# Kernel optimization log

Measured on AMD Instinct MI355X. Metric: run time of the kernel, lower is better.

## Reference

```python
import jax, jax.numpy as jnp
import numpy as np

B, T, C, H, W = 16, 8, 16, 64, 64
HID = 32          # round(sqrt(num_audio_input_ch * num_latent_ch)) = sqrt(16*64)
LAT = 64          # num_latent_ch
K = 3             # kernel_size


def conv(x, w, b):
    # x: [B,Cin,H,W], w: [Cout,Cin,K,K] (OIHW), SAME padding == padding (1,1) for 3x3
    y = jax.lax.conv_general_dilated(x, w, (1, 1), 'SAME',
                                     dimension_numbers=('NCHW', 'OIHW', 'NCHW'))
    return y + b[None, :, None, None]


def lstm_scan(x_seq, w, b, hid):
    # x_seq: [T,B,Cin,H,W] -> hidden sequence [T,B,hid,H,W]
    Bn, Hh, Ww = x_seq.shape[1], x_seq.shape[3], x_seq.shape[4]
    h0 = jnp.zeros((Bn, hid, Hh, Ww), x_seq.dtype)

    def step(carry, x_t):
        h, c = carry
        z = conv(jnp.concatenate([x_t, h], axis=1), w, b)     # [B,4*hid,H,W]
        i, f, o, g = jnp.split(z, 4, axis=1)                   # gate order i,f,o,g
        c2 = jax.nn.sigmoid(f) * c + jax.nn.sigmoid(i) * jnp.tanh(g)
        h2 = jax.nn.sigmoid(o) * jnp.tanh(c2)
        return (h2, c2), h2

    _, hs = jax.lax.scan(step, (h0, h0), x_seq)
    return hs


def bidir_layer(x_seq, wf, bf, wb, bb, hid):
    hf = lstm_scan(x_seq, wf, bf, hid)
    hb = jnp.flip(lstm_scan(jnp.flip(x_seq, 0), wb, bb, hid), 0)
    return jnp.concatenate([hf, hb], axis=2)                   # [T,B,2*hid,H,W]


def setup_inputs() -> dict:
    key = jax.random.key(0)
    ks = jax.random.split(key, 16)
    s = 0.05
    pe_dim = C * H * W
    inp = {
        'x_audio': jax.random.normal(ks[0], (B, T, C, H, W), jnp.float32),
        'midi_notes': jax.random.uniform(ks[1], (B, T, 2), jnp.float32, 0.0, 127.0),
        # note encoder: Linear(2,4) -> ReLU -> Linear(4, C*H*W) -> Tanh
        'enc_w1': jax.random.normal(ks[2], (2, 4), jnp.float32) * s,
        'enc_b1': jnp.zeros((4,), jnp.float32),
        'enc_w2': jax.random.normal(ks[3], (4, pe_dim), jnp.float32) * s,
        'enc_b2': jnp.zeros((pe_dim,), jnp.float32),
        # layer 0 (input C=16), fwd + bwd cells
        'w0f': jax.random.normal(ks[4], (4 * HID, C + HID, K, K), jnp.float32) * s,
        'b0f': jnp.zeros((4 * HID,), jnp.float32),
        'w0b': jax.random.normal(ks[5], (4 * HID, C + HID, K, K), jnp.float32) * s,
        'b0b': jnp.zeros((4 * HID,), jnp.float32),
        # layer 1 (input 2*HID=64)
        'w1f': jax.random.normal(ks[6], (4 * HID, 2 * HID + HID, K, K), jnp.float32) * s,
        'b1f': jnp.zeros((4 * HID,), jnp.float32),
        'w1b': jax.random.normal(ks[7], (4 * HID, 2 * HID + HID, K, K), jnp.float32) * s,
        'b1b': jnp.zeros((4 * HID,), jnp.float32),
        # final conv: 2*HID -> LAT
        'fc_w': jax.random.normal(ks[8], (LAT, 2 * HID, K, K), jnp.float32) * s,
        'fc_b': jnp.zeros((LAT,), jnp.float32),
    }
    return inp


def reference(x_audio, midi_notes, enc_w1, enc_b1, enc_w2, enc_b2,
              w0f, b0f, w0b, b0b, w1f, b1f, w1b, b1b, fc_w, fc_b):
    # positional encoding from MIDI notes, vectorized over all timesteps
    notes = -0.5 + midi_notes / 64.0                              # [B,T,2]
    pe = jnp.tanh(jax.nn.relu(notes @ enc_w1 + enc_b1) @ enc_w2 + enc_b2)  # [B,T,C*H*W]
    x = x_audio + pe.reshape(x_audio.shape)
    xs = jnp.transpose(x, (1, 0, 2, 3, 4))                        # [T,B,C,H,W]
    h = bidir_layer(xs, w0f, b0f, w0b, b0b, HID)                  # [T,B,64,H,W]
    h = bidir_layer(h, w1f, b1f, w1b, b1b, HID)                   # [T,B,64,H,W]
    return conv(h[-1], fc_w, fc_b)                                # [B,LAT,H,W]
```

## Files before the change

### kernel.cpp

```cpp
#include <hip/hip_runtime.h>

typedef _Float16 f16;
typedef _Float16 f16x8 __attribute__((ext_vector_type(8)));
typedef float f32x16 __attribute__((ext_vector_type(16)));

namespace {

constexpr int B_ = 16, T_ = 8, HW = 4096;

__device__ __forceinline__ float sigm(float x)  { return 1.f / (1.f + __expf(-x)); }
__device__ __forceinline__ float ftanh(float x) { return 1.f - 2.f / (1.f + __expf(2.f * x)); }

__device__ __forceinline__ f32x16 zero16() {
  f32x16 v;
#pragma unroll
  for (int i = 0; i < 16; ++i) v[i] = 0.f;
  return v;
}

struct WSet { const float* src; f16* dst; int KC, NCO, CIN; };

__global__ void warr_kernel(WSet s0, WSet s1, WSet s2, WSet s3, WSet s4) {
  WSet s = s0;
  switch (blockIdx.y) { case 1: s = s1; break; case 2: s = s2; break;
                        case 3: s = s3; break; case 4: s = s4; break; default: break; }
  int n = 9 * s.KC * s.NCO * 16;
  int i = blockIdx.x * 256 + threadIdx.x;
  if (i >= n) return;
  int kk = i & 15;
  int t = i >> 4;
  int co = t % s.NCO;
  int dkc = t / s.NCO;
  int kc = dkc % s.KC, dydx = dkc / s.KC;
  int ci = kc * 16 + kk;
  float v = (ci < s.CIN) ? s.src[(co * s.CIN + ci) * 9 + dydx] : 0.f;
  s.dst[i] = (f16)v;
}

__global__ void pe_kernel(const float* __restrict__ xa, const float* __restrict__ midi,
                          const float* __restrict__ w1, const float* __restrict__ b1,
                          const float* __restrict__ w2, const float* __restrict__ b2,
                          f16* __restrict__ xs) {
  int gid = blockIdx.x * 256 + threadIdx.x;
  int half = gid & 1;
  int gpx = gid >> 1;
  int bt = gpx >> 12, gp = gpx & 4095;
  float n0 = -0.5f + midi[bt * 2 + 0] * (1.f / 64.f);
  float n1 = -0.5f + midi[bt * 2 + 1] * (1.f / 64.f);
  float hk[4];
#pragma unroll
  for (int k = 0; k < 4; ++k)
    hk[k] = fmaxf(fmaf(n0, w1[k], fmaf(n1, w1[4 + k], b1[k])), 0.f);
  f16x8 ov;
#pragma unroll
  for (int j = 0; j < 8; ++j) {
    int c = half * 8 + j;
    long p = (long)c * HW + gp;
    float z = b2[p];
#pragma unroll
    for (int k = 0; k < 4; ++k) z = fmaf(hk[k], w2[(long)k * 65536 + p], z);
    ov[j] = (f16)(xa[(long)bt * 65536 + p] + ftanh(z));
  }
  *reinterpret_cast<f16x8*>(xs + (long)gpx * 16 + half * 8) = ov;
}

struct ConvDir {
  const f16* x;  long xbs;
  const f16* h;  long hbs;
  const f16* w;
  const float* bias;
  const float* cin;
  float* cout;
  f16* hout; long hobs;
};

template<int CIN1, int CIN2, int CINPAD, int KCF, int KC, int HST, int HOST,
         bool GATES, int NCO, int MG, int MFRAG>
__global__ __launch_bounds__(512, 4)
void conv_mfma(ConvDir p0, ConvDir p1)
{
  constexpr int NG = 8 / MG;
  constexpr int NF = NCO / (NG * 32);
  constexpr int ACT_BYTES = 180 * CINPAD * 2;
  constexpr int ZB_BYTES  = GATES ? 64 * 128 * 4 : 0;
  constexpr int SMEM = ACT_BYTES > ZB_BYTES ? ACT_BYTES : ZB_BYTES;
  __shared__ __align__(16) char smem[SMEM];
  f16*   act  = (f16*)smem;
  float* zbuf = (float*)smem;

  const ConvDir P = blockIdx.y ? p1 : p0;
  const int b = blockIdx.z;
  const int tileY = blockIdx.x >> 2, tileX = blockIdx.x & 3;
  const int gy0 = tileY * 8, gx0 = tileX * 16;
  const int tid = threadIdx.x;

  constexpr int UPX = CIN1 / 8, UPH = CIN2 / 8, UPP = UPX + UPH;
  const bool have_h = (P.h != nullptr);
  for (int i = tid; i < 180 * UPP; i += 512) {
    int px = i / UPP, u = i - px * UPP;
    if (u >= UPX && !have_h) continue;
    int py = px / 18, pxx = px - py * 18;
    int gy = gy0 + py - 1, gx = gx0 + pxx - 1;
    f16x8 v;
#pragma unroll
    for (int j = 0; j < 8; ++j) v[j] = (f16)0.f;
    if ((unsigned)gy < 64u && (unsigned)gx < 64u) {
      long gp = (long)gy * 64 + gx;
      const f16* src = (u < UPX) ? (P.x + b * P.xbs + gp * CIN1 + u * 8)
                                 : (P.h + b * P.hbs + gp * HST + (u - UPX) * 8);
      v = *reinterpret_cast<const f16x8*>(src);
    }
    *reinterpret_cast<f16x8*>(act + px * CINPAD + u * 8) = v;
  }
  __syncthreads();

  const int lane = tid & 63, wv = tid >> 6;
  const int mg = wv % MG, ng = wv / MG;
  const int rl = lane & 31;
  const int khalf = (lane >> 5) * 8;
  const int laneA = ((rl >> 4) * 18 + (rl & 15)) * CINPAD + khalf;
  const int laneB = rl * 16 + khalf;

  f32x16 acc[MFRAG][NF];
#pragma unroll
  for (int m = 0; m < MFRAG; ++m)
#pragma unroll
    for (int nf = 0; nf < NF; ++nf) acc[m][nf] = zero16();

  const f16* __restrict__ wng = P.w + laneB;
  const f16* __restrict__ arow = act + laneA;

#pragma unroll
  for (int dy = 0; dy < 3; ++dy)
#pragma unroll
  for (int dx = 0; dx < 3; ++dx) {
    const int dydx = dy * 3 + dx;
    f16x8 bf[KC][NF];
#pragma unroll
    for (int kc = 0; kc < KC; ++kc)
#pragma unroll
      for (int nf = 0; nf < NF; ++nf)
        bf[kc][nf] = *reinterpret_cast<const f16x8*>(
            wng + ((long)(dydx * KCF + kc) * NCO + (ng * NF + nf) * 32) * 16);
    f16x8 af[MFRAG][KC];
#pragma unroll
    for (int m = 0; m < MFRAG; ++m)
#pragma unroll
      for (int kc = 0; kc < KC; ++kc)
        af[m][kc] = *reinterpret_cast<const f16x8*>(
            arow + dx * CINPAD + (((mg * MFRAG + m) * 2 + dy) * 18) * CINPAD + kc * 16);
#pragma unroll
    for (int kc = 0; kc < KC; ++kc)
#pragma unroll
      for (int m = 0; m < MFRAG; ++m)
#pragma unroll
        for (int nf = 0; nf < NF; ++nf)
          acc[m][nf] = __builtin_amdgcn_mfma_f32_32x32x16_f16(af[m][kc], bf[kc][nf], acc[m][nf], 0, 0, 0);
  }

  __syncthreads();

  if constexpr (GATES) {
#pragma unroll
    for (int phase = 0; phase < 2; ++phase) {
      if (mg == phase) {
#pragma unroll
        for (int m = 0; m < MFRAG; ++m) {
#pragma unroll
          for (int nf = 0; nf < NF; ++nf) {
            const int col = (ng * NF + nf) * 32 + rl;
            const float bs = P.bias[col];
#pragma unroll
            for (int r = 0; r < 16; ++r) {
              int row = (r & 3) + 8 * (r >> 2) + 4 * (lane >> 5);
              zbuf[(m * 32 + row) * 128 + col] = acc[m][nf][r] + bs;
            }
          }
        }
      }
      __syncthreads();
      const int hid = tid & 31;
#pragma unroll
      for (int i = 0; i < 4; ++i) {
        int pl = (tid >> 5) + i * 16;
        int pxt = phase * 64 + pl;
        int py = pxt >> 4, pxx = pxt & 15;
        long gp = (long)(gy0 + py) * 64 + (gx0 + pxx);
        float zi = zbuf[pl * 128 + hid];
        float zf = zbuf[pl * 128 + 32 + hid];
        float zo = zbuf[pl * 128 + 64 + hid];
        float zg = zbuf[pl * 128 + 96 + hid];
        long cidx = ((long)b * HW + gp) * 32 + hid;
        float cp = P.cin ? P.cin[cidx] : 0.f;
        float c2 = sigm(zf) * cp + sigm(zi) * ftanh(zg);
        P.cout[cidx] = c2;
        P.hout[b * P.hobs + gp * HOST + hid] = (f16)(sigm(zo) * ftanh(c2));
      }
      __syncthreads();
    }
  } else {
#pragma unroll
    for (int m = 0; m < MFRAG; ++m) {
#pragma unroll
      for (int nf = 0; nf < NF; ++nf) {
        const int co = (ng * NF + nf) * 32 + rl;
        const float bs = P.bias[co];
#pragma unroll
        for (int r = 0; r < 16; ++r) {
          int row = (r & 3) + 8 * (r >> 2) + 4 * (lane >> 5);
          int pxt = (mg * MFRAG + m) * 32 + row;
          int py = pxt >> 4, pxx = pxt & 15;
          long gp = (long)(gy0 + py) * 64 + (gx0 + pxx);
          P.cout[((long)b * NCO + co) * HW + gp] = acc[m][nf][r] + bs;
        }
      }
    }
  }
}

}

extern "C" void kernel_launch(void* const* d_in, const int* in_sizes, int n_in,
                              void* d_out, int out_size, void* d_ws, size_t ws_size,
                              hipStream_t stream) {
  const float* x_audio = (const float*)d_in[0];
  const float* midi    = (const float*)d_in[1];
  const float* enc_w1  = (const float*)d_in[2];
  const float* enc_b1  = (const float*)d_in[3];
  const float* enc_w2  = (const float*)d_in[4];
  const float* enc_b2  = (const float*)d_in[5];
  const float* w0f = (const float*)d_in[6];
  const float* b0f = (const float*)d_in[7];
  const float* w0b = (const float*)d_in[8];
  const float* b0b = (const float*)d_in[9];
  const float* w1f = (const float*)d_in[10];
  const float* b1f = (const float*)d_in[11];
  const float* w1b = (const float*)d_in[12];
  const float* b1b = (const float*)d_in[13];
  const float* fcw = (const float*)d_in[14];
  const float* fcb = (const float*)d_in[15];

  char* ws = (char*)d_ws;
  size_t off = 0;
  auto alloc = [&](size_t bytes) { char* p = ws + off; off += (bytes + 255) & ~(size_t)255; return p; };

  f16* xs    = (f16*)alloc((size_t)B_ * T_ * HW * 16 * 2);
  f16* seq0  = (f16*)alloc((size_t)T_ * B_ * HW * 64 * 2);
  float* c0f = (float*)alloc((size_t)B_ * HW * 32 * 4);
  float* c0b = (float*)alloc((size_t)B_ * HW * 32 * 4);
  float* c1f = (float*)alloc((size_t)B_ * HW * 32 * 4);
  float* c1bw= (float*)alloc((size_t)B_ * HW * 32 * 4);
  f16* h1p0  = (f16*)alloc((size_t)B_ * HW * 32 * 2);
  f16* h1p1  = (f16*)alloc((size_t)B_ * HW * 32 * 2);
  f16* h1bw  = (f16*)alloc((size_t)B_ * HW * 32 * 2);
  f16* wt0f  = (f16*)alloc((size_t)9 * 3 * 128 * 16 * 2);
  f16* wt0b  = (f16*)alloc((size_t)9 * 3 * 128 * 16 * 2);
  f16* wt1f  = (f16*)alloc((size_t)9 * 6 * 128 * 16 * 2);
  f16* wt1b  = (f16*)alloc((size_t)9 * 6 * 128 * 16 * 2);
  f16* wtfc  = (f16*)alloc((size_t)9 * 4 * 64 * 16 * 2);

  {
    WSet s0{w0f, wt0f, 3, 128, 48}, s1{w0b, wt0b, 3, 128, 48};
    WSet s2{w1f, wt1f, 6, 128, 96}, s3{w1b, wt1b, 6, 128, 96};
    WSet s4{fcw, wtfc, 4, 64, 64};
    warr_kernel<<<dim3(432, 5), 256, 0, stream>>>(s0, s1, s2, s3, s4);
  }

  pe_kernel<<<(B_ * T_ * HW * 2) / 256, 256, 0, stream>>>(
      x_audio, midi, enc_w1, enc_b1, enc_w2, enc_b2, xs);

  const long XSB  = (long)T_ * HW * 16;
  const long SLAB = (long)B_ * HW * 64;
  const long SB   = (long)HW * 64;
  const long HB   = (long)HW * 32;

  {
    ConvDir f{xs, XSB, nullptr, SB, wt0f, b0f, nullptr, c0f, seq0, SB};
    ConvDir r{xs + (long)7 * HW * 16, XSB, nullptr, SB, wt0b, b0b, nullptr, c0b,
              seq0 + (long)7 * SLAB + 32, SB};
    conv_mfma<16, 32, 56, 3, 1, 64, 64, true, 128, 2, 2>
        <<<dim3(32, 2, 16), 512, 0, stream>>>(f, r);
  }
  for (int s = 1; s < 8; ++s) {
    int tf = s, tb = 7 - s;
    ConvDir f{xs + (long)tf * HW * 16, XSB,
              seq0 + (long)(tf - 1) * SLAB, SB,
              wt0f, b0f, c0f, c0f,
              seq0 + (long)tf * SLAB, SB};
    ConvDir r{xs + (long)tb * HW * 16, XSB,
              seq0 + (long)(tb + 1) * SLAB + 32, SB,
              wt0b, b0b, c0b, c0b,
              seq0 + (long)tb * SLAB + 32, SB};
    conv_mfma<16, 32, 56, 3, 3, 64, 64, true, 128, 2, 2>
        <<<dim3(32, 2, 16), 512, 0, stream>>>(f, r);
  }

  {
    ConvDir f{seq0, SB, nullptr, HB, wt1f, b1f, nullptr, c1f, h1p0, HB};
    ConvDir r{seq0 + 7 * SLAB, SB, nullptr, HB, wt1b, b1b, nullptr, c1bw, h1bw, HB};
    conv_mfma<64, 32, 104, 6, 4, 32, 32, true, 128, 2, 2>
        <<<dim3(32, 2, 16), 512, 0, stream>>>(f, r);
  }
  for (int s = 1; s < 8; ++s) {
    f16* hprev = (s & 1) ? h1p0 : h1p1;
    f16* hcur  = (s & 1) ? h1p1 : h1p0;
    ConvDir f{seq0 + (long)s * SLAB, SB, hprev, HB, wt1f, b1f, c1f, c1f, hcur, HB};
    conv_mfma<64, 32, 104, 6, 6, 32, 32, true, 128, 2, 2>
        <<<dim3(32, 1, 16), 512, 0, stream>>>(f, f);
  }

  {
    ConvDir f{h1p1, HB, h1bw, HB, wtfc, fcb, nullptr, (float*)d_out, nullptr, 0};
    conv_mfma<32, 32, 72, 4, 4, 32, 32, false, 64, 4, 1>
        <<<dim3(32, 1, 16), 512, 0, stream>>>(f, f);
  }
}
```

Before: 516.7 us.

## Software-pipeline conv MFMA loop with register double-buffering and early weight prefetch

Restructures the conv kernel main loop into phases over (tap, K-chunk) with double-buffered A/B fragments in registers, so the next phase's LDS and global weight loads overlap the current MFMAs. Global activation loads are issued into registers before the first weight prefetch, then written to LDS, hiding load latency. The gate epilogue now stages pre-activations in fp16 LDS in a single pass instead of two fp32 phases, which removes extra barriers. The cost is higher register pressure, and rounding the gate inputs to fp16 loses precision.

```diff
diff --git a/kernel.cpp b/kernel.cpp
--- a/kernel.cpp
+++ b/kernel.cpp
@@ -15,6 +15,13 @@
   f32x16 v;
 #pragma unroll
   for (int i = 0; i < 16; ++i) v[i] = 0.f;
+  return v;
+}
+
+__device__ __forceinline__ f16x8 zero8h() {
+  f16x8 v;
+#pragma unroll
+  for (int i = 0; i < 8; ++i) v[i] = (f16)0.f;
   return v;
 }
 
@@ -74,45 +81,26 @@
   f16* hout; long hobs;
 };
 
-template<int CIN1, int CIN2, int CINPAD, int KCF, int KC, int HST, int HOST,
+template<int CIN1, int CIN2, int CINPAD, int KCF, int KC, int CH, int HST, int HOST,
          bool GATES, int NCO, int MG, int MFRAG>
 __global__ __launch_bounds__(512, 4)
 void conv_mfma(ConvDir p0, ConvDir p1)
 {
   constexpr int NG = 8 / MG;
-  constexpr int NF = NCO / (NG * 32);
+  constexpr int NCH = KC / CH;
+  constexpr int NPH = 9 * NCH;
   constexpr int ACT_BYTES = 180 * CINPAD * 2;
-  constexpr int ZB_BYTES  = GATES ? 64 * 128 * 4 : 0;
+  constexpr int ZB_BYTES  = GATES ? 128 * 128 * 2 : 0;
   constexpr int SMEM = ACT_BYTES > ZB_BYTES ? ACT_BYTES : ZB_BYTES;
   __shared__ __align__(16) char smem[SMEM];
-  f16*   act  = (f16*)smem;
-  float* zbuf = (float*)smem;
+  f16* act = (f16*)smem;
+  f16* zls = (f16*)smem;
 
   const ConvDir P = blockIdx.y ? p1 : p0;
   const int b = blockIdx.z;
   const int tileY = blockIdx.x >> 2, tileX = blockIdx.x & 3;
   const int gy0 = tileY * 8, gx0 = tileX * 16;
   const int tid = threadIdx.x;
-
-  constexpr int UPX = CIN1 / 8, UPH = CIN2 / 8, UPP = UPX + UPH;
-  const bool have_h = (P.h != nullptr);
-  for (int i = tid; i < 180 * UPP; i += 512) {
-    int px = i / UPP, u = i - px * UPP;
-    if (u >= UPX && !have_h) continue;
-    int py = px / 18, pxx = px - py * 18;
-    int gy = gy0 + py - 1, gx = gx0 + pxx - 1;
-    f16x8 v;
-#pragma unroll
-    for (int j = 0; j < 8; ++j) v[j] = (f16)0.f;
-    if ((unsigned)gy < 64u && (unsigned)gx < 64u) {
-      long gp = (long)gy * 64 + gx;
-      const f16* src = (u < UPX) ? (P.x + b * P.xbs + gp * CIN1 + u * 8)
-                                 : (P.h + b * P.hbs + gp * HST + (u - UPX) * 8);
-      v = *reinterpret_cast<const f16x8*>(src);
-    }
-    *reinterpret_cast<f16x8*>(act + px * CINPAD + u * 8) = v;
-  }
-  __syncthreads();
 
   const int lane = tid & 63, wv = tid >> 6;
   const int mg = wv % MG, ng = wv / MG;
@@ -120,99 +108,128 @@
   const int khalf = (lane >> 5) * 8;
   const int laneA = ((rl >> 4) * 18 + (rl & 15)) * CINPAD + khalf;
   const int laneB = rl * 16 + khalf;
-
-  f32x16 acc[MFRAG][NF];
-#pragma unroll
-  for (int m = 0; m < MFRAG; ++m)
-#pragma unroll
-    for (int nf = 0; nf < NF; ++nf) acc[m][nf] = zero16();
-
-  const f16* __restrict__ wng = P.w + laneB;
+  const f16* __restrict__ wng = P.w + laneB + (long)ng * 32 * 16;
   const f16* __restrict__ arow = act + laneA;
 
-#pragma unroll
-  for (int dy = 0; dy < 3; ++dy)
-#pragma unroll
-  for (int dx = 0; dx < 3; ++dx) {
-    const int dydx = dy * 3 + dx;
-    f16x8 bf[KC][NF];
-#pragma unroll
-    for (int kc = 0; kc < KC; ++kc)
-#pragma unroll
-      for (int nf = 0; nf < NF; ++nf)
-        bf[kc][nf] = *reinterpret_cast<const f16x8*>(
-            wng + ((long)(dydx * KCF + kc) * NCO + (ng * NF + nf) * 32) * 16);
-    f16x8 af[MFRAG][KC];
+  constexpr int UPX = CIN1 / 8, UPH = CIN2 / 8, UPP = UPX + UPH;
+  constexpr int NU  = 180 * UPP;
+  constexpr int PER = (NU + 511) / 512;
+  const bool have_h = (P.h != nullptr);
+  f16x8 sreg[PER];
+#pragma unroll
+  for (int p = 0; p < PER; ++p) {
+    sreg[p] = zero8h();
+    int i = tid + p * 512;
+    if (i < NU) {
+      int px = i / UPP, u = i - px * UPP;
+      int py = px / 18, pxx = px - py * 18;
+      int gy = gy0 + py - 1, gx = gx0 + pxx - 1;
+      if ((unsigned)gy < 64u && (unsigned)gx < 64u && (u < UPX || have_h)) {
+        long gp = (long)gy * 64 + gx;
+        const f16* src = (u < UPX) ? (P.x + b * P.xbs + gp * CIN1 + u * 8)
+                                   : (P.h + b * P.hbs + gp * HST + (u - UPX) * 8);
+        sreg[p] = *reinterpret_cast<const f16x8*>(src);
+      }
+    }
+  }
+
+  f16x8 bfr[2][CH];
+  f16x8 afr[2][MFRAG][CH];
+
+  auto LBF = [&](int ph) {
+    const int slot = ph & 1;
+    const int dydx = ph / NCH, kc0 = (ph % NCH) * CH;
+#pragma unroll
+    for (int c = 0; c < CH; ++c)
+      bfr[slot][c] = *reinterpret_cast<const f16x8*>(
+          wng + (long)(dydx * KCF + kc0 + c) * NCO * 16);
+  };
+  auto LAF = [&](int ph) {
+    const int slot = ph & 1;
+    const int dydx = ph / NCH, kc0 = (ph % NCH) * CH;
+    const int dy = dydx / 3, dx = dydx % 3;
 #pragma unroll
     for (int m = 0; m < MFRAG; ++m)
 #pragma unroll
-      for (int kc = 0; kc < KC; ++kc)
-        af[m][kc] = *reinterpret_cast<const f16x8*>(
-            arow + dx * CINPAD + (((mg * MFRAG + m) * 2 + dy) * 18) * CINPAD + kc * 16);
-#pragma unroll
-    for (int kc = 0; kc < KC; ++kc)
+      for (int c = 0; c < CH; ++c)
+        afr[slot][m][c] = *reinterpret_cast<const f16x8*>(
+            arow + dx * CINPAD + (((mg * MFRAG + m) * 2 + dy) * 18) * CINPAD
+            + (kc0 + c) * 16);
+  };
+
+  LBF(0);
+  if (NPH > 1) LBF(1);
+
+#pragma unroll
+  for (int p = 0; p < PER; ++p) {
+    int i = tid + p * 512;
+    if (i < NU) {
+      int px = i / UPP, u = i - px * UPP;
+      *reinterpret_cast<f16x8*>(act + px * CINPAD + u * 8) = sreg[p];
+    }
+  }
+  __syncthreads();
+
+  f32x16 acc[MFRAG];
+#pragma unroll
+  for (int m = 0; m < MFRAG; ++m) acc[m] = zero16();
+
+  LAF(0);
+#pragma unroll
+  for (int ph = 0; ph < NPH; ++ph) {
+    const int slot = ph & 1;
+    if (ph + 1 < NPH) LAF(ph + 1);
+#pragma unroll
+    for (int c = 0; c < CH; ++c)
 #pragma unroll
       for (int m = 0; m < MFRAG; ++m)
-#pragma unroll
-        for (int nf = 0; nf < NF; ++nf)
-          acc[m][nf] = __builtin_amdgcn_mfma_f32_32x32x16_f16(af[m][kc], bf[kc][nf], acc[m][nf], 0, 0, 0);
+        acc[m] = __builtin_amdgcn_mfma_f32_32x32x16_f16(afr[slot][m][c], bfr[slot][c], acc[m], 0, 0, 0);
+    if (ph + 2 < NPH) LBF(ph + 2);
   }
 
   __syncthreads();
 
   if constexpr (GATES) {
-#pragma unroll
-    for (int phase = 0; phase < 2; ++phase) {
-      if (mg == phase) {
-#pragma unroll
-        for (int m = 0; m < MFRAG; ++m) {
-#pragma unroll
-          for (int nf = 0; nf < NF; ++nf) {
-            const int col = (ng * NF + nf) * 32 + rl;
-            const float bs = P.bias[col];
-#pragma unroll
-            for (int r = 0; r < 16; ++r) {
-              int row = (r & 3) + 8 * (r >> 2) + 4 * (lane >> 5);
-              zbuf[(m * 32 + row) * 128 + col] = acc[m][nf][r] + bs;
-            }
-          }
-        }
+    const int col = ng * 32 + rl;
+    const float bs = P.bias[col];
+#pragma unroll
+    for (int m = 0; m < MFRAG; ++m) {
+#pragma unroll
+      for (int r = 0; r < 16; ++r) {
+        int row = (r & 3) + 8 * (r >> 2) + 4 * (lane >> 5);
+        int px = (mg * MFRAG + m) * 32 + row;
+        zls[px * 128 + col] = (f16)(acc[m][r] + bs);
       }
-      __syncthreads();
-      const int hid = tid & 31;
-#pragma unroll
-      for (int i = 0; i < 4; ++i) {
-        int pl = (tid >> 5) + i * 16;
-        int pxt = phase * 64 + pl;
+    }
+    __syncthreads();
+#pragma unroll
+    for (int i = 0; i < 8; ++i) {
+      int idx = tid + i * 512;
+      int hid = idx & 31, px = idx >> 5;
+      float zi = (float)zls[px * 128 + hid];
+      float zf = (float)zls[px * 128 + 32 + hid];
+      float zo = (float)zls[px * 128 + 64 + hid];
+      float zg = (float)zls[px * 128 + 96 + hid];
+      int py = px >> 4, pxx = px & 15;
+      long gp = (long)(gy0 + py) * 64 + (gx0 + pxx);
+      long cidx = ((long)b * HW + gp) * 32 + hid;
+      float cp = P.cin ? P.cin[cidx] : 0.f;
+      float c2 = sigm(zf) * cp + sigm(zi) * ftanh(zg);
+      P.cout[cidx] = c2;
+      P.hout[b * P.hobs + gp * HOST + hid] = (f16)(sigm(zo) * ftanh(c2));
+    }
+  } else {
+    const int co = ng * 32 + rl;
+    const float bs = P.bias[co];
+#pragma unroll
+    for (int m = 0; m < MFRAG; ++m) {
+#pragma unroll
+      for (int r = 0; r < 16; ++r) {
+        int row = (r & 3) + 8 * (r >> 2) + 4 * (lane >> 5);
+        int pxt = (mg * MFRAG + m) * 32 + row;
         int py = pxt >> 4, pxx = pxt & 15;
         long gp = (long)(gy0 + py) * 64 + (gx0 + pxx);
-        float zi = zbuf[pl * 128 + hid];
-        float zf = zbuf[pl * 128 + 32 + hid];
-        float zo = zbuf[pl * 128 + 64 + hid];
-        float zg = zbuf[pl * 128 + 96 + hid];
-        long cidx = ((long)b * HW + gp) * 32 + hid;
-        float cp = P.cin ? P.cin[cidx] : 0.f;
-        float c2 = sigm(zf) * cp + sigm(zi) * ftanh(zg);
-        P.cout[cidx] = c2;
-        P.hout[b * P.hobs + gp * HOST + hid] = (f16)(sigm(zo) * ftanh(c2));
-      }
-      __syncthreads();
-    }
-  } else {
-#pragma unroll
-    for (int m = 0; m < MFRAG; ++m) {
-#pragma unroll
-      for (int nf = 0; nf < NF; ++nf) {
-        const int co = (ng * NF + nf) * 32 + rl;
-        const float bs = P.bias[co];
-#pragma unroll
-        for (int r = 0; r < 16; ++r) {
-          int row = (r & 3) + 8 * (r >> 2) + 4 * (lane >> 5);
-          int pxt = (mg * MFRAG + m) * 32 + row;
-          int py = pxt >> 4, pxx = pxt & 15;
-          long gp = (long)(gy0 + py) * 64 + (gx0 + pxx);
-          P.cout[((long)b * NCO + co) * HW + gp] = acc[m][nf][r] + bs;
-        }
+        P.cout[((long)b * NCO + co) * HW + gp] = acc[m][r] + bs;
       }
     }
   }
@@ -278,7 +295,7 @@
     ConvDir f{xs, XSB, nullptr, SB, wt0f, b0f, nullptr, c0f, seq0, SB};
     ConvDir r{xs + (long)7 * HW * 16, XSB, nullptr, SB, wt0b, b0b, nullptr, c0b,
               seq0 + (long)7 * SLAB + 32, SB};
-    conv_mfma<16, 32, 56, 3, 1, 64, 64, true, 128, 2, 2>
+    conv_mfma<16, 32, 56, 3, 1, 1, 64, 64, true, 128, 2, 2>
         <<<dim3(32, 2, 16), 512, 0, stream>>>(f, r);
   }
   for (int s = 1; s < 8; ++s) {
@@ -291,27 +308,27 @@
               seq0 + (long)(tb + 1) * SLAB + 32, SB,
               wt0b, b0b, c0b, c0b,
               seq0 + (long)tb * SLAB + 32, SB};
-    conv_mfma<16, 32, 56, 3, 3, 64, 64, true, 128, 2, 2>
+    conv_mfma<16, 32, 56, 3, 3, 3, 64, 64, true, 128, 2, 2>
         <<<dim3(32, 2, 16), 512, 0, stream>>>(f, r);
   }
 
   {
     ConvDir f{seq0, SB, nullptr, HB, wt1f, b1f, nullptr, c1f, h1p0, HB};
     ConvDir r{seq0 + 7 * SLAB, SB, nullptr, HB, wt1b, b1b, nullptr, c1bw, h1bw, HB};
-    conv_mfma<64, 32, 104, 6, 4, 32, 32, true, 128, 2, 2>
+    conv_mfma<64, 32, 104, 6, 4, 2, 32, 32, true, 128, 2, 2>
         <<<dim3(32, 2, 16), 512, 0, stream>>>(f, r);
   }
   for (int s = 1; s < 8; ++s) {
     f16* hprev = (s & 1) ? h1p0 : h1p1;
     f16* hcur  = (s & 1) ? h1p1 : h1p0;
     ConvDir f{seq0 + (long)s * SLAB, SB, hprev, HB, wt1f, b1f, c1f, c1f, hcur, HB};
-    conv_mfma<64, 32, 104, 6, 6, 32, 32, true, 128, 2, 2>
+    conv_mfma<64, 32, 104, 6, 6, 3, 32, 32, true, 128, 2, 2>
         <<<dim3(32, 1, 16), 512, 0, stream>>>(f, f);
   }
 
   {
     ConvDir f{h1p1, HB, h1bw, HB, wtfc, fcb, nullptr, (float*)d_out, nullptr, 0};
-    conv_mfma<32, 32, 72, 4, 4, 32, 32, false, 64, 4, 1>
+    conv_mfma<32, 32, 72, 4, 4, 2, 32, 32, false, 64, 4, 1>
         <<<dim3(32, 1, 16), 512, 0, stream>>>(f, f);
   }
 }
```

New measurement: 499.4 us. -3.3%, faster.
